# Optimization experiments

Measured on AMD Instinct MI355X. Metric: run time of the kernel, lower is better.

## Reference

```python
import jax, jax.numpy as jnp
import numpy as np

CLARITY_K, CLARITY_SIGMA = 31, 8.0
TEXTURE_K, TEXTURE_SIGMA = 7, 1.5


def _gauss1d(size, sigma):
    grid = np.arange(size, dtype=np.float32) - size // 2
    g = np.exp(-grid ** 2 / (2.0 * sigma * sigma))
    return (g / g.sum()).astype(np.float32)


def _blur(img, g1d):
    # Separable Gaussian blur: the original 2D kernel is the outer product of
    # the normalized 1D gaussian with itself, so two 1D passes are exact.
    size = g1d.shape[0]
    pad = size // 2
    kh = jnp.asarray(g1d, img.dtype).reshape(1, 1, size, 1)  # OIHW, vertical
    kw = jnp.asarray(g1d, img.dtype).reshape(1, 1, 1, size)  # OIHW, horizontal
    dn = jax.lax.conv_dimension_numbers(img.shape, kh.shape, ('NCHW', 'OIHW', 'NCHW'))
    y = jax.lax.conv_general_dilated(img, kh, (1, 1), [(pad, pad), (0, 0)], dimension_numbers=dn)
    y = jax.lax.conv_general_dilated(y, kw, (1, 1), [(0, 0), (pad, pad)], dimension_numbers=dn)
    return y


def setup_inputs() -> dict:
    key = jax.random.key(0)
    kx, kc, kt = jax.random.split(key, 3)
    x = jax.random.uniform(kx, (8, 3, 1024, 1024), dtype=jnp.float32)
    clarity = jax.random.normal(kc, (), dtype=jnp.float32)
    texture = jax.random.normal(kt, (), dtype=jnp.float32)
    return {"x": x, "clarity": clarity, "texture": texture}


def reference(x, clarity, texture):
    g_clar = _gauss1d(CLARITY_K, CLARITY_SIGMA)
    g_tex = _gauss1d(TEXTURE_K, TEXTURE_SIGMA)

    # Rec.709 luma, shape [B,1,H,W]
    luma = 0.2126 * x[:, 0:1] + 0.7152 * x[:, 1:2] + 0.0722 * x[:, 2:3]

    mid_freq = luma - _blur(luma, g_clar)    # 31x31 gaussian
    high_freq = luma - _blur(luma, g_tex)    # 7x7 gaussian

    clarity_amount = jnp.tanh(clarity) * 0.5
    texture_amount = jnp.tanh(texture) * 0.3

    luma_enhanced = luma + clarity_amount * mid_freq + texture_amount * high_freq
    ratio = (luma_enhanced + 1e-6) / (luma + 1e-6)
    return jnp.clip(x * ratio, 0.0, 1.0)
```

## Files before the change

### kernel.cpp

```cpp
#include <hip/hip_runtime.h>
#include <hip/hip_fp16.h>
#include <cmath>

#define HH   1024
#define WW   1024
#define HW   (HH * WW)

#define SW    64
#define TH    64
#define T31R  94
#define T7R   70
#define NIT   6
#define SPX   96
#define SOFF  16
#define UPR   24

constexpr double cexp(double v) {
    double term = 1.0, sum = 1.0;
    for (int i = 1; i < 64; ++i) { term *= v / (double)i; sum += term; }
    return sum;
}
struct GW { float g31[31]; float g7[7]; };
constexpr GW make_gw() {
    GW r{};
    double t31[31]; double s31 = 0.0;
    for (int i = 0; i < 31; ++i) { double d = (double)(i - 15); t31[i] = cexp(-d * d / 128.0); s31 += t31[i]; }
    for (int i = 0; i < 31; ++i) r.g31[i] = (float)(t31[i] / s31);
    double t7[7]; double s7 = 0.0;
    for (int i = 0; i < 7; ++i) { double d = (double)(i - 3); t7[i] = cexp(-d * d / 4.5); s7 += t7[i]; }
    for (int i = 0; i < 7; ++i) r.g7[i] = (float)(t7[i] / s7);
    return r;
}
__constant__ GW GWC = make_gw();

__global__ __launch_bounds__(256, 4)
void fused_tile(const float* __restrict__ x,
                const float* __restrict__ clar,
                const float* __restrict__ tex,
                float* __restrict__ out) {
    __shared__ __align__(16) __half t31s [T31R][SW];
    __shared__ __align__(16) __half t7s  [T7R][SW];
    __shared__ __align__(16) __half stage[4][4][SPX];

    const int id    = blockIdx.x;
    const int xcd   = id & 7;
    const int j8    = id >> 3;
    const int combo = j8 & 127;
    const int sub   = j8 >> 7;
    const int band  = xcd * 2 + sub;
    const int img   = combo >> 4;
    const int strip = combo & 15;

    const int y0 = band * TH;
    const int x0 = strip * SW;
    const int t  = threadIdx.x;
    const int w    = t >> 6;
    const int lane = t & 63;

    const float* xb = x   + (size_t)img * 3 * HW;
    float*       ob = out + (size_t)img * 3 * HW;

    const int r0s = lane / UPR;
    const int c0s = lane - UPR * r0s;
    const int u1  = lane + 64;
    const int r1r = u1 / UPR;
    const int r1s = r1r > 3 ? 3 : r1r;
    const int c1s = u1 - UPR * r1r;
    const int col0 = x0 - SOFF + 4 * c0s;
    const int col1 = x0 - SOFF + 4 * c1s;
    const int col0c = col0 < 0 ? 0 : (col0 > WW - 4 ? WW - 4 : col0);
    const int col1c = col1 < 0 ? 0 : (col1 > WW - 4 ? WW - 4 : col1);
    const float cm0 = ((unsigned)col0 < (unsigned)WW) ? 1.f : 0.f;
    const float cm1 = ((unsigned)col1 < (unsigned)WW) ? 1.f : 0.f;

    float4 R0, G0, B0, R1, G1, B1;
    float  mk0, mk1;

    auto issue = [&](int it) {
        const int gbase = it * 16;
        {
            const int tr = gbase + 4 * w + r0s;
            const int y  = y0 - 15 + tr;
            const int yc = y < 0 ? 0 : (y > HH - 1 ? HH - 1 : y);
            mk0 = (tr < T31R && (unsigned)y < (unsigned)HH) ? cm0 : 0.f;
            const float* xr = xb + (size_t)yc * WW + col0c;
            R0 = *(const float4*)(xr);
            G0 = *(const float4*)(xr + HW);
            B0 = *(const float4*)(xr + 2 * HW);
        }
        {
            const int tr = gbase + 4 * w + r1s;
            const int y  = y0 - 15 + tr;
            const int yc = y < 0 ? 0 : (y > HH - 1 ? HH - 1 : y);
            mk1 = (tr < T31R && (unsigned)y < (unsigned)HH) ? cm1 : 0.f;
            const float* xr = xb + (size_t)yc * WW + col1c;
            R1 = *(const float4*)(xr);
            G1 = *(const float4*)(xr + HW);
            B1 = *(const float4*)(xr + 2 * HW);
        }
    };

    issue(0);
    __builtin_amdgcn_sched_barrier(0);

    for (int it = 0; it < NIT; ++it) {
        {
            union { float2 f; __half2 h[2]; } W;
            W.h[0] = __floats2half2_rn(mk0 * fmaf(0.2126f, R0.x, fmaf(0.7152f, G0.x, 0.0722f * B0.x)),
                                       mk0 * fmaf(0.2126f, R0.y, fmaf(0.7152f, G0.y, 0.0722f * B0.y)));
            W.h[1] = __floats2half2_rn(mk0 * fmaf(0.2126f, R0.z, fmaf(0.7152f, G0.z, 0.0722f * B0.z)),
                                       mk0 * fmaf(0.2126f, R0.w, fmaf(0.7152f, G0.w, 0.0722f * B0.w)));
            *(float2*)&stage[w][r0s][4 * c0s] = W.f;
            union { float2 f; __half2 h[2]; } V;
            V.h[0] = __floats2half2_rn(mk1 * fmaf(0.2126f, R1.x, fmaf(0.7152f, G1.x, 0.0722f * B1.x)),
                                       mk1 * fmaf(0.2126f, R1.y, fmaf(0.7152f, G1.y, 0.0722f * B1.y)));
            V.h[1] = __floats2half2_rn(mk1 * fmaf(0.2126f, R1.z, fmaf(0.7152f, G1.z, 0.0722f * B1.z)),
                                       mk1 * fmaf(0.2126f, R1.w, fmaf(0.7152f, G1.w, 0.0722f * B1.w)));
            *(float2*)&stage[w][r1s][4 * c1s] = V.f;
        }

        if (it + 1 < NIT) {
            issue(it + 1);
        }
        __builtin_amdgcn_sched_barrier(0);

        {
            const int lr = (t >> 4) & 3;
            const int c  = t & 15;
            const int tr = it * 16 + (t >> 4);
            if (tr < T31R) {
                float win[36];
                #pragma unroll
                for (int q = 0; q < 9; ++q) {
                    union { float2 f; __half2 h[2]; } U;
                    U.f = *(const float2*)&stage[w][lr][4 * c + 4 * q];
                    const float2 a = __half22float2(U.h[0]);
                    const float2 b = __half22float2(U.h[1]);
                    win[4 * q]     = a.x; win[4 * q + 1] = a.y;
                    win[4 * q + 2] = b.x; win[4 * q + 3] = b.y;
                }
                float o[4] = {0.f, 0.f, 0.f, 0.f};
                float p[4] = {0.f, 0.f, 0.f, 0.f};
                #pragma unroll
                for (int s = 0; s < 31; ++s) {
                    const float g = GWC.g31[s];
                    o[0] = fmaf(g, win[1 + s], o[0]);
                    o[1] = fmaf(g, win[2 + s], o[1]);
                    o[2] = fmaf(g, win[3 + s], o[2]);
                    o[3] = fmaf(g, win[4 + s], o[3]);
                }
                #pragma unroll
                for (int s = 0; s < 7; ++s) {
                    const float g = GWC.g7[s];
                    p[0] = fmaf(g, win[13 + s], p[0]);
                    p[1] = fmaf(g, win[14 + s], p[1]);
                    p[2] = fmaf(g, win[15 + s], p[2]);
                    p[3] = fmaf(g, win[16 + s], p[3]);
                }
                union { float2 f; __half2 h[2]; } W;
                W.h[0] = __floats2half2_rn(o[0], o[1]);
                W.h[1] = __floats2half2_rn(o[2], o[3]);
                *(float2*)&t31s[tr][4 * c] = W.f;
                if (tr >= 12 && tr < 12 + T7R) {
                    union { float2 f; __half2 h[2]; } V;
                    V.h[0] = __floats2half2_rn(p[0], p[1]);
                    V.h[1] = __floats2half2_rn(p[2], p[3]);
                    *(float2*)&t7s[tr - 12][4 * c] = V.f;
                }
            }
        }
    }

    __syncthreads();

    const float ca = tanhf(clar[0]) * 0.5f;
    const float ta = tanhf(tex[0]) * 0.3f;

    const int rg = t >> 4;
    const int r0 = rg * 4;
    const int cc = 4 * (t & 15);

    const float* p0 = xb + (size_t)(y0 + r0) * WW + x0 + cc;
    float4 R  = *(const float4*)(p0);
    float4 G  = *(const float4*)(p0 + HW);
    float4 Bc = *(const float4*)(p0 + 2 * HW);
    __builtin_amdgcn_sched_barrier(0);

    #pragma unroll
    for (int j = 0; j < 4; ++j) {
        float4 Rn, Gn, Bn;
        if (j < 3) {
            const float* pn = xb + (size_t)(y0 + r0 + j + 1) * WW + x0 + cc;
            Rn = *(const float4*)(pn);
            Gn = *(const float4*)(pn + HW);
            Bn = *(const float4*)(pn + 2 * HW);
        }
        __builtin_amdgcn_sched_barrier(0);

        float4 a31 = make_float4(0.f, 0.f, 0.f, 0.f);
        #pragma unroll
        for (int q = 0; q < 31; ++q) {
            union { float2 f; __half2 h[2]; } U;
            U.f = *(const float2*)&t31s[r0 + j + q][cc];
            const float2 a = __half22float2(U.h[0]);
            const float2 b = __half22float2(U.h[1]);
            const float g = GWC.g31[q];
            a31.x = fmaf(g, a.x, a31.x);
            a31.y = fmaf(g, a.y, a31.y);
            a31.z = fmaf(g, b.x, a31.z);
            a31.w = fmaf(g, b.y, a31.w);
        }
        float4 a7 = make_float4(0.f, 0.f, 0.f, 0.f);
        #pragma unroll
        for (int q = 0; q < 7; ++q) {
            union { float2 f; __half2 h[2]; } U;
            U.f = *(const float2*)&t7s[r0 + j + q][cc];
            const float2 a = __half22float2(U.h[0]);
            const float2 b = __half22float2(U.h[1]);
            const float g = GWC.g7[q];
            a7.x = fmaf(g, a.x, a7.x);
            a7.y = fmaf(g, a.y, a7.y);
            a7.z = fmaf(g, b.x, a7.z);
            a7.w = fmaf(g, b.y, a7.w);
        }

        const int y = y0 + r0 + j;
        float* qo = ob + (size_t)y * WW + x0 + cc;

        float4 o0, o1, o2;
        {
            const float L0 = fmaf(0.2126f, R.x, fmaf(0.7152f, G.x, 0.0722f * Bc.x));
            const float L1 = fmaf(0.2126f, R.y, fmaf(0.7152f, G.y, 0.0722f * Bc.y));
            const float L2 = fmaf(0.2126f, R.z, fmaf(0.7152f, G.z, 0.0722f * Bc.z));
            const float L3 = fmaf(0.2126f, R.w, fmaf(0.7152f, G.w, 0.0722f * Bc.w));
            const float e0 = L0 + ca * (L0 - a31.x) + ta * (L0 - a7.x);
            const float e1 = L1 + ca * (L1 - a31.y) + ta * (L1 - a7.y);
            const float e2 = L2 + ca * (L2 - a31.z) + ta * (L2 - a7.z);
            const float e3 = L3 + ca * (L3 - a31.w) + ta * (L3 - a7.w);
            const float r0r = (e0 + 1e-6f) * __builtin_amdgcn_rcpf(L0 + 1e-6f);
            const float r1r = (e1 + 1e-6f) * __builtin_amdgcn_rcpf(L1 + 1e-6f);
            const float r2r = (e2 + 1e-6f) * __builtin_amdgcn_rcpf(L2 + 1e-6f);
            const float r3r = (e3 + 1e-6f) * __builtin_amdgcn_rcpf(L3 + 1e-6f);
            o0.x = fminf(fmaxf(R.x  * r0r, 0.f), 1.f);
            o0.y = fminf(fmaxf(R.y  * r1r, 0.f), 1.f);
            o0.z = fminf(fmaxf(R.z  * r2r, 0.f), 1.f);
            o0.w = fminf(fmaxf(R.w  * r3r, 0.f), 1.f);
            o1.x = fminf(fmaxf(G.x  * r0r, 0.f), 1.f);
            o1.y = fminf(fmaxf(G.y  * r1r, 0.f), 1.f);
            o1.z = fminf(fmaxf(G.z  * r2r, 0.f), 1.f);
            o1.w = fminf(fmaxf(G.w  * r3r, 0.f), 1.f);
            o2.x = fminf(fmaxf(Bc.x * r0r, 0.f), 1.f);
            o2.y = fminf(fmaxf(Bc.y * r1r, 0.f), 1.f);
            o2.z = fminf(fmaxf(Bc.z * r2r, 0.f), 1.f);
            o2.w = fminf(fmaxf(Bc.w * r3r, 0.f), 1.f);
        }
        *(float4*)(qo)          = o0;
        *(float4*)(qo + HW)     = o1;
        *(float4*)(qo + 2 * HW) = o2;

        if (j < 3) { R = Rn; G = Gn; Bc = Bn; }
    }
}

extern "C" void kernel_launch(void* const* d_in, const int* in_sizes, int n_in,
                              void* d_out, int out_size, void* d_ws, size_t ws_size,
                              hipStream_t stream) {
    const float* x    = (const float*)d_in[0];
    const float* clar = (const float*)d_in[1];
    const float* tex  = (const float*)d_in[2];
    float* out = (float*)d_out;

    dim3 grid(8 * 16 * 16);
    dim3 block(256);
    hipLaunchKernelGGL(fused_tile, grid, block, 0, stream, x, clar, tex, out);
}
```

Baseline: 200.6 us.

## Store luma and 31-tap intermediates in fp32 LDS and share vertical taps across rows

Switches the staging buffer and the 31-tap horizontal intermediate from half to float in LDS, which removes the half conversions and doubles their LDS footprint. The vertical pass is restructured so each LDS row read is reused across the four output rows a thread owns, cutting LDS reads from 4x31 to 34 for the wide blur and from 4x7 to 10 for the narrow one. The software prefetch of the next row's RGB in the epilogue is dropped, and the pixels are loaded just before use. The larger LDS (about 31 KB versus about 21 KB per block) may lower occupancy against the launch bound of 4 blocks, and the accumulators raise register pressure.

```diff
diff --git a/kernel.cpp b/kernel.cpp
--- a/kernel.cpp
+++ b/kernel.cpp
@@ -38,9 +38,9 @@
                 const float* __restrict__ clar,
                 const float* __restrict__ tex,
                 float* __restrict__ out) {
-    __shared__ __align__(16) __half t31s [T31R][SW];
+    __shared__ __align__(16) float  t31s [T31R][SW];
     __shared__ __align__(16) __half t7s  [T7R][SW];
-    __shared__ __align__(16) __half stage[4][4][SPX];
+    __shared__ __align__(16) float  stage[4][4][SPX];
 
     const int id    = blockIdx.x;
     const int xcd   = id & 7;
@@ -105,23 +105,21 @@
 
     for (int it = 0; it < NIT; ++it) {
         {
-            union { float2 f; __half2 h[2]; } W;
-            W.h[0] = __floats2half2_rn(mk0 * fmaf(0.2126f, R0.x, fmaf(0.7152f, G0.x, 0.0722f * B0.x)),
-                                       mk0 * fmaf(0.2126f, R0.y, fmaf(0.7152f, G0.y, 0.0722f * B0.y)));
-            W.h[1] = __floats2half2_rn(mk0 * fmaf(0.2126f, R0.z, fmaf(0.7152f, G0.z, 0.0722f * B0.z)),
-                                       mk0 * fmaf(0.2126f, R0.w, fmaf(0.7152f, G0.w, 0.0722f * B0.w)));
-            *(float2*)&stage[w][r0s][4 * c0s] = W.f;
-            union { float2 f; __half2 h[2]; } V;
-            V.h[0] = __floats2half2_rn(mk1 * fmaf(0.2126f, R1.x, fmaf(0.7152f, G1.x, 0.0722f * B1.x)),
-                                       mk1 * fmaf(0.2126f, R1.y, fmaf(0.7152f, G1.y, 0.0722f * B1.y)));
-            V.h[1] = __floats2half2_rn(mk1 * fmaf(0.2126f, R1.z, fmaf(0.7152f, G1.z, 0.0722f * B1.z)),
-                                       mk1 * fmaf(0.2126f, R1.w, fmaf(0.7152f, G1.w, 0.0722f * B1.w)));
-            *(float2*)&stage[w][r1s][4 * c1s] = V.f;
-        }
-
-        if (it + 1 < NIT) {
-            issue(it + 1);
-        }
+            float4 L0;
+            L0.x = mk0 * fmaf(0.2126f, R0.x, fmaf(0.7152f, G0.x, 0.0722f * B0.x));
+            L0.y = mk0 * fmaf(0.2126f, R0.y, fmaf(0.7152f, G0.y, 0.0722f * B0.y));
+            L0.z = mk0 * fmaf(0.2126f, R0.z, fmaf(0.7152f, G0.z, 0.0722f * B0.z));
+            L0.w = mk0 * fmaf(0.2126f, R0.w, fmaf(0.7152f, G0.w, 0.0722f * B0.w));
+            *(float4*)&stage[w][r0s][4 * c0s] = L0;
+            float4 L1;
+            L1.x = mk1 * fmaf(0.2126f, R1.x, fmaf(0.7152f, G1.x, 0.0722f * B1.x));
+            L1.y = mk1 * fmaf(0.2126f, R1.y, fmaf(0.7152f, G1.y, 0.0722f * B1.y));
+            L1.z = mk1 * fmaf(0.2126f, R1.z, fmaf(0.7152f, G1.z, 0.0722f * B1.z));
+            L1.w = mk1 * fmaf(0.2126f, R1.w, fmaf(0.7152f, G1.w, 0.0722f * B1.w));
+            *(float4*)&stage[w][r1s][4 * c1s] = L1;
+        }
+
+        if (it + 1 < NIT) issue(it + 1);
         __builtin_amdgcn_sched_barrier(0);
 
         {
@@ -132,12 +130,9 @@
                 float win[36];
                 #pragma unroll
                 for (int q = 0; q < 9; ++q) {
-                    union { float2 f; __half2 h[2]; } U;
-                    U.f = *(const float2*)&stage[w][lr][4 * c + 4 * q];
-                    const float2 a = __half22float2(U.h[0]);
-                    const float2 b = __half22float2(U.h[1]);
-                    win[4 * q]     = a.x; win[4 * q + 1] = a.y;
-                    win[4 * q + 2] = b.x; win[4 * q + 3] = b.y;
+                    const float4 u = *(const float4*)&stage[w][lr][4 * c + 4 * q];
+                    win[4 * q]     = u.x; win[4 * q + 1] = u.y;
+                    win[4 * q + 2] = u.z; win[4 * q + 3] = u.w;
                 }
                 float o[4] = {0.f, 0.f, 0.f, 0.f};
                 float p[4] = {0.f, 0.f, 0.f, 0.f};
@@ -157,10 +152,7 @@
                     p[2] = fmaf(g, win[15 + s], p[2]);
                     p[3] = fmaf(g, win[16 + s], p[3]);
                 }
-                union { float2 f; __half2 h[2]; } W;
-                W.h[0] = __floats2half2_rn(o[0], o[1]);
-                W.h[1] = __floats2half2_rn(o[2], o[3]);
-                *(float2*)&t31s[tr][4 * c] = W.f;
+                *(float4*)&t31s[tr][4 * c] = make_float4(o[0], o[1], o[2], o[3]);
                 if (tr >= 12 && tr < 12 + T7R) {
                     union { float2 f; __half2 h[2]; } V;
                     V.h[0] = __floats2half2_rn(p[0], p[1]);
@@ -180,85 +172,87 @@
     const int r0 = rg * 4;
     const int cc = 4 * (t & 15);
 
-    const float* p0 = xb + (size_t)(y0 + r0) * WW + x0 + cc;
-    float4 R  = *(const float4*)(p0);
-    float4 G  = *(const float4*)(p0 + HW);
-    float4 Bc = *(const float4*)(p0 + 2 * HW);
-    __builtin_amdgcn_sched_barrier(0);
-
+    float4 a31[4];
+    float4 a7[4];
     #pragma unroll
     for (int j = 0; j < 4; ++j) {
-        float4 Rn, Gn, Bn;
-        if (j < 3) {
-            const float* pn = xb + (size_t)(y0 + r0 + j + 1) * WW + x0 + cc;
-            Rn = *(const float4*)(pn);
-            Gn = *(const float4*)(pn + HW);
-            Bn = *(const float4*)(pn + 2 * HW);
-        }
-        __builtin_amdgcn_sched_barrier(0);
-
-        float4 a31 = make_float4(0.f, 0.f, 0.f, 0.f);
+        a31[j] = make_float4(0.f, 0.f, 0.f, 0.f);
+        a7[j]  = make_float4(0.f, 0.f, 0.f, 0.f);
+    }
+
+    #pragma unroll
+    for (int q = 0; q < 34; ++q) {
+        const float4 tap = *(const float4*)&t31s[r0 + q][cc];
         #pragma unroll
-        for (int q = 0; q < 31; ++q) {
-            union { float2 f; __half2 h[2]; } U;
-            U.f = *(const float2*)&t31s[r0 + j + q][cc];
-            const float2 a = __half22float2(U.h[0]);
-            const float2 b = __half22float2(U.h[1]);
-            const float g = GWC.g31[q];
-            a31.x = fmaf(g, a.x, a31.x);
-            a31.y = fmaf(g, a.y, a31.y);
-            a31.z = fmaf(g, b.x, a31.z);
-            a31.w = fmaf(g, b.y, a31.w);
-        }
-        float4 a7 = make_float4(0.f, 0.f, 0.f, 0.f);
+        for (int j = 0; j < 4; ++j) {
+            const int s = q - j;
+            if (s >= 0 && s <= 30) {
+                const float g = GWC.g31[s];
+                a31[j].x = fmaf(g, tap.x, a31[j].x);
+                a31[j].y = fmaf(g, tap.y, a31[j].y);
+                a31[j].z = fmaf(g, tap.z, a31[j].z);
+                a31[j].w = fmaf(g, tap.w, a31[j].w);
+            }
+        }
+    }
+    #pragma unroll
+    for (int q = 0; q < 10; ++q) {
+        union { float2 f; __half2 h[2]; } U;
+        U.f = *(const float2*)&t7s[r0 + q][cc];
+        const float2 a = __half22float2(U.h[0]);
+        const float2 b = __half22float2(U.h[1]);
         #pragma unroll
-        for (int q = 0; q < 7; ++q) {
-            union { float2 f; __half2 h[2]; } U;
-            U.f = *(const float2*)&t7s[r0 + j + q][cc];
-            const float2 a = __half22float2(U.h[0]);
-            const float2 b = __half22float2(U.h[1]);
-            const float g = GWC.g7[q];
-            a7.x = fmaf(g, a.x, a7.x);
-            a7.y = fmaf(g, a.y, a7.y);
-            a7.z = fmaf(g, b.x, a7.z);
-            a7.w = fmaf(g, b.y, a7.w);
-        }
-
+        for (int j = 0; j < 4; ++j) {
+            const int s = q - j;
+            if (s >= 0 && s <= 6) {
+                const float g = GWC.g7[s];
+                a7[j].x = fmaf(g, a.x, a7[j].x);
+                a7[j].y = fmaf(g, a.y, a7[j].y);
+                a7[j].z = fmaf(g, b.x, a7[j].z);
+                a7[j].w = fmaf(g, b.y, a7[j].w);
+            }
+        }
+    }
+
+    #pragma unroll
+    for (int j = 0; j < 4; ++j) {
         const int y = y0 + r0 + j;
+        const float* px = xb + (size_t)y * WW + x0 + cc;
+        const float4 R  = *(const float4*)(px);
+        const float4 G  = *(const float4*)(px + HW);
+        const float4 Bc = *(const float4*)(px + 2 * HW);
+
+        const float L0 = fmaf(0.2126f, R.x, fmaf(0.7152f, G.x, 0.0722f * Bc.x));
+        const float L1 = fmaf(0.2126f, R.y, fmaf(0.7152f, G.y, 0.0722f * Bc.y));
+        const float L2 = fmaf(0.2126f, R.z, fmaf(0.7152f, G.z, 0.0722f * Bc.z));
+        const float L3 = fmaf(0.2126f, R.w, fmaf(0.7152f, G.w, 0.0722f * Bc.w));
+        const float e0 = L0 + ca * (L0 - a31[j].x) + ta * (L0 - a7[j].x);
+        const float e1 = L1 + ca * (L1 - a31[j].y) + ta * (L1 - a7[j].y);
+        const float e2 = L2 + ca * (L2 - a31[j].z) + ta * (L2 - a7[j].z);
+        const float e3 = L3 + ca * (L3 - a31[j].w) + ta * (L3 - a7[j].w);
+        const float r0r = (e0 + 1e-6f) * __builtin_amdgcn_rcpf(L0 + 1e-6f);
+        const float r1r = (e1 + 1e-6f) * __builtin_amdgcn_rcpf(L1 + 1e-6f);
+        const float r2r = (e2 + 1e-6f) * __builtin_amdgcn_rcpf(L2 + 1e-6f);
+        const float r3r = (e3 + 1e-6f) * __builtin_amdgcn_rcpf(L3 + 1e-6f);
+
+        float4 o0, o1, o2;
+        o0.x = fminf(fmaxf(R.x  * r0r, 0.f), 1.f);
+        o0.y = fminf(fmaxf(R.y  * r1r, 0.f), 1.f);
+        o0.z = fminf(fmaxf(R.z  * r2r, 0.f), 1.f);
+        o0.w = fminf(fmaxf(R.w  * r3r, 0.f), 1.f);
+        o1.x = fminf(fmaxf(G.x  * r0r, 0.f), 1.f);
+        o1.y = fminf(fmaxf(G.y  * r1r, 0.f), 1.f);
+        o1.z = fminf(fmaxf(G.z  * r2r, 0.f), 1.f);
+        o1.w = fminf(fmaxf(G.w  * r3r, 0.f), 1.f);
+        o2.x = fminf(fmaxf(Bc.x * r0r, 0.f), 1.f);
+        o2.y = fminf(fmaxf(Bc.y * r1r, 0.f), 1.f);
+        o2.z = fminf(fmaxf(Bc.z * r2r, 0.f), 1.f);
+        o2.w = fminf(fmaxf(Bc.w * r3r, 0.f), 1.f);
+
         float* qo = ob + (size_t)y * WW + x0 + cc;
-
-        float4 o0, o1, o2;
-        {
-            const float L0 = fmaf(0.2126f, R.x, fmaf(0.7152f, G.x, 0.0722f * Bc.x));
-            const float L1 = fmaf(0.2126f, R.y, fmaf(0.7152f, G.y, 0.0722f * Bc.y));
-            const float L2 = fmaf(0.2126f, R.z, fmaf(0.7152f, G.z, 0.0722f * Bc.z));
-            const float L3 = fmaf(0.2126f, R.w, fmaf(0.7152f, G.w, 0.0722f * Bc.w));
-            const float e0 = L0 + ca * (L0 - a31.x) + ta * (L0 - a7.x);
-            const float e1 = L1 + ca * (L1 - a31.y) + ta * (L1 - a7.y);
-            const float e2 = L2 + ca * (L2 - a31.z) + ta * (L2 - a7.z);
-            const float e3 = L3 + ca * (L3 - a31.w) + ta * (L3 - a7.w);
-            const float r0r = (e0 + 1e-6f) * __builtin_amdgcn_rcpf(L0 + 1e-6f);
-            const float r1r = (e1 + 1e-6f) * __builtin_amdgcn_rcpf(L1 + 1e-6f);
-            const float r2r = (e2 + 1e-6f) * __builtin_amdgcn_rcpf(L2 + 1e-6f);
-            const float r3r = (e3 + 1e-6f) * __builtin_amdgcn_rcpf(L3 + 1e-6f);
-            o0.x = fminf(fmaxf(R.x  * r0r, 0.f), 1.f);
-            o0.y = fminf(fmaxf(R.y  * r1r, 0.f), 1.f);
-            o0.z = fminf(fmaxf(R.z  * r2r, 0.f), 1.f);
-            o0.w = fminf(fmaxf(R.w  * r3r, 0.f), 1.f);
-            o1.x = fminf(fmaxf(G.x  * r0r, 0.f), 1.f);
-            o1.y = fminf(fmaxf(G.y  * r1r, 0.f), 1.f);
-            o1.z = fminf(fmaxf(G.z  * r2r, 0.f), 1.f);
-            o1.w = fminf(fmaxf(G.w  * r3r, 0.f), 1.f);
-            o2.x = fminf(fmaxf(Bc.x * r0r, 0.f), 1.f);
-            o2.y = fminf(fmaxf(Bc.y * r1r, 0.f), 1.f);
-            o2.z = fminf(fmaxf(Bc.z * r2r, 0.f), 1.f);
-            o2.w = fminf(fmaxf(Bc.w * r3r, 0.f), 1.f);
-        }
         *(float4*)(qo)          = o0;
         *(float4*)(qo + HW)     = o1;
         *(float4*)(qo + 2 * HW) = o2;
-
-        if (j < 3) { R = Rn; G = Gn; Bc = Bn; }
     }
 }
 
```

Result: slower. 357.3 us (+78.1%).
